# Optimization experiments

Hardware: AMD Instinct MI355X
Metric: run time of the kernel (lower is better)

## Reference

```python
import jax, jax.numpy as jnp
import numpy as np

OMODE, PMODE, NZ = 2, 4, 8
NY = NX = 512
NPY = NPX = 128
NPOS = 1024
BATCH = 64


def setup_inputs() -> dict:
    key = jax.random.key(0)
    ks = jax.random.split(key, 8)
    obja = jax.random.uniform(ks[0], (OMODE, NZ, NY, NX), jnp.float32, 0.9, 1.0)
    objp = 0.1 * jax.random.normal(ks[1], (OMODE, NZ, NY, NX), jnp.float32)
    probe = jax.random.normal(ks[2], (PMODE, NPY, NPX, 2), jnp.float32)
    probe_pos_shifts = 0.5 * jax.random.normal(ks[3], (NPOS, 2), jnp.float32)
    theta = jax.random.normal(ks[4], (NPY, NPX), jnp.float32)
    H = jnp.stack([jnp.cos(theta), jnp.sin(theta)], axis=-1)  # unit-modulus Fresnel phasor (re, im)
    omode_occu = jax.nn.softmax(jax.random.normal(ks[5], (OMODE,), jnp.float32))
    indices = jax.random.randint(ks[6], (BATCH,), 0, NPOS, jnp.int32)
    crop_pos = jax.random.randint(ks[7], (NPOS, 2), 0, NY - NPY, jnp.int32)
    return {"obja": obja, "objp": objp, "probe": probe,
            "probe_pos_shifts": probe_pos_shifts, "H": H, "omode_occu": omode_occu,
            "indices": indices, "crop_pos": crop_pos}


def reference(obja, objp, probe, probe_pos_shifts, H, omode_occu, indices, crop_pos):
    npy, npx = probe.shape[1], probe.shape[2]
    probe_c = probe[..., 0] + 1j * probe[..., 1]   # (pmode, Npy, Npx) complex64
    H_c = H[..., 0] + 1j * H[..., 1]               # (Npy, Npx) complex64

    # --- indexed patch gather: (omode, nz, N, Npy, Npx) -> (N, omode, nz, Npy, Npx) ---
    cy = crop_pos[indices, 0]
    cx = crop_pos[indices, 1]
    gy = cy[:, None, None] + jnp.arange(npy, dtype=jnp.int32)[None, :, None]  # (N, Npy, 1)
    gx = cx[:, None, None] + jnp.arange(npx, dtype=jnp.int32)[None, None, :]  # (N, 1, Npx)
    pa = jnp.transpose(obja[:, :, gy, gx], (2, 0, 1, 3, 4))
    pp = jnp.transpose(objp[:, :, gy, gx], (2, 0, 1, 3, 4))
    T = pa * jnp.exp(1j * pp)  # transmission per slice, (N, omode, nz, Npy, Npx)

    # --- sub-pixel Fourier probe shifts (imshift_batch) ---
    kpy = jnp.fft.fftfreq(npy).astype(jnp.float32)
    kpx = jnp.fft.fftfreq(npx).astype(jnp.float32)
    sh = probe_pos_shifts[indices]  # (N, 2)
    ramp = jnp.exp(-2j * jnp.pi * (kpy[None, :, None] * sh[:, 0, None, None]
                                   + kpx[None, None, :] * sh[:, 1, None, None]))  # (N, Npy, Npx)
    probes = jnp.fft.ifft2(jnp.fft.fft2(probe_c)[None] * ramp[:, None])  # (N, pmode, Npy, Npx)

    # --- multislice propagation: psi (N, omode, pmode, Npy, Npx) ---
    psi = probes[:, None]
    nz = T.shape[2]
    for z in range(nz):
        psi = psi * T[:, :, z, None]
        if z < nz - 1:
            psi = jnp.fft.ifft2(jnp.fft.fft2(psi) * H_c)

    # --- far-field detector intensity, mode-incoherent sum ---
    dp = jnp.einsum('o,nopyx->nyx', omode_occu, jnp.abs(jnp.fft.fft2(psi)) ** 2)
    return dp
```

## Files before the change

### kernel.cpp

```cpp
#include <hip/hip_runtime.h>

static constexpr int OMODE = 2, PMODE = 4, NZ = 8;
static constexpr int NYX = 512;
static constexpr int NP  = 128;
static constexpr int BATCH = 64;
static constexpr int LSTR = 129;
static constexpr float INV_N2 = 1.0f / 16384.0f;

typedef float v2f __attribute__((ext_vector_type(2)));

__device__ __forceinline__ int br7(int x) { return (int)(__brev((unsigned)x) >> 25); }

__device__ __forceinline__ v2f splat2(float s) { return (v2f){s, s}; }
__device__ __forceinline__ v2f swapv(v2f v) { return __builtin_shufflevector(v, v, 1, 0); }
__device__ __forceinline__ v2f cmulv(v2f a, float br_, float bi_) {
  return a * splat2(br_) + swapv(a) * (v2f){-bi_, bi_};
}
__device__ __forceinline__ v2f cmulvv(v2f a, v2f b) {
  return a * splat2(b.x) + swapv(a) * (v2f){-b.y, b.y};
}

template<int CTRL>
__device__ __forceinline__ float dppf(float x) {
  int i = __float_as_int(x);
  int r = __builtin_amdgcn_update_dpp(i, i, CTRL, 0xF, 0xF, false);
  return __int_as_float(r);
}

struct Tw {
  float tc6, ts6;
  float g[6];
  float dwr[6], dwi[6];
};

template<int CTRL, int S>
__device__ __forceinline__ v2f bfly_dpp(v2f m, const Tw& tw) {
  v2f t = (v2f){dppf<CTRL>(m.x), dppf<CTRL>(m.y)};
  return t + splat2(tw.g[S]) * m;
}
template<int OFS, int S>
__device__ __forceinline__ v2f bfly_swz(v2f m, const Tw& tw) {
  v2f t;
  t.x = __int_as_float(__builtin_amdgcn_ds_swizzle(__float_as_int(m.x), OFS));
  t.y = __int_as_float(__builtin_amdgcn_ds_swizzle(__float_as_int(m.y), OFS));
  return t + splat2(tw.g[S]) * m;
}
__device__ __forceinline__ v2f bfly_bp32(v2f m, int bp32, float g5) {
  v2f t;
  t.x = __int_as_float(__builtin_amdgcn_ds_bpermute(bp32, __float_as_int(m.x)));
  t.y = __int_as_float(__builtin_amdgcn_ds_bpermute(bp32, __float_as_int(m.y)));
  return t + splat2(g5) * m;
}

template<int S> __device__ __forceinline__ v2f twd(v2f d, const Tw& tw) {
  return d * splat2(tw.dwr[S]) + swapv(d) * (v2f){-tw.dwi[S], tw.dwi[S]};
}
template<int S> __device__ __forceinline__ v2f twc(v2f a, const Tw& tw) {
  return a * splat2(tw.dwr[S]) + swapv(a) * (v2f){tw.dwi[S], -tw.dwi[S]};
}

__device__ __forceinline__ void dif128(v2f& A, v2f& B, const Tw& tw, int bp32) {
  {
    v2f d = A - B;
    A = A + B;
    B = d * splat2(tw.tc6) + swapv(d) * (v2f){tw.ts6, -tw.ts6};
  }
  A = twd<5>(bfly_bp32(A, bp32, tw.g[5]), tw);  B = twd<5>(bfly_bp32(B, bp32, tw.g[5]), tw);
  A = twd<4>(bfly_swz<0x401F, 4>(A, tw), tw);   B = twd<4>(bfly_swz<0x401F, 4>(B, tw), tw);
  A = twd<3>(bfly_swz<0x201F, 3>(A, tw), tw);   B = twd<3>(bfly_swz<0x201F, 3>(B, tw), tw);
  A = twd<2>(bfly_swz<0x101F, 2>(A, tw), tw);   B = twd<2>(bfly_swz<0x101F, 2>(B, tw), tw);
  A = twd<1>(bfly_dpp<0x4E, 1>(A, tw), tw);     B = twd<1>(bfly_dpp<0x4E, 1>(B, tw), tw);
  A = bfly_dpp<0xB1, 0>(A, tw);                 B = bfly_dpp<0xB1, 0>(B, tw);
}

__device__ __forceinline__ void dit128(v2f& A, v2f& B, const Tw& tw, int bp32) {
  A = bfly_dpp<0xB1, 0>(A, tw);                 B = bfly_dpp<0xB1, 0>(B, tw);
  A = bfly_dpp<0x4E, 1>(twc<1>(A, tw), tw);     B = bfly_dpp<0x4E, 1>(twc<1>(B, tw), tw);
  A = bfly_swz<0x101F, 2>(twc<2>(A, tw), tw);   B = bfly_swz<0x101F, 2>(twc<2>(B, tw), tw);
  A = bfly_swz<0x201F, 3>(twc<3>(A, tw), tw);   B = bfly_swz<0x201F, 3>(twc<3>(B, tw), tw);
  A = bfly_swz<0x401F, 4>(twc<4>(A, tw), tw);   B = bfly_swz<0x401F, 4>(twc<4>(B, tw), tw);
  A = bfly_bp32(twc<5>(A, tw), bp32, tw.g[5]);  B = bfly_bp32(twc<5>(B, tw), bp32, tw.g[5]);
  {
    v2f m = B * splat2(tw.tc6) + swapv(B) * (v2f){-tw.ts6, tw.ts6};
    B = A - m;
    A = A + m;
  }
}

__global__ void __launch_bounds__(256) init_hpre(const float* __restrict__ H,
                                                 float2* __restrict__ hp) {
  int i = blockIdx.x * blockDim.x + threadIdx.x;
  if (i >= NP * NP) return;
  int px = i >> 7, py = i & (NP - 1);
  int ky = br7(py), kx = br7(px);
  hp[px * NP + py] = make_float2(H[(ky * NP + kx) * 2 + 0] * INV_N2,
                                 H[(ky * NP + kx) * 2 + 1] * INV_N2);
}

__global__ void __launch_bounds__(256) init_ramp(const float* __restrict__ shifts,
                                                 const int* __restrict__ indices,
                                                 float2* __restrict__ rampy,
                                                 float2* __restrict__ rampx) {
  int i = blockIdx.x * blockDim.x + threadIdx.x;
  if (i >= 2 * BATCH * NP) return;
  int which = (i >= BATCH * NP) ? 1 : 0;
  int r = i - which * BATCH * NP;
  int n = r >> 7, slot = r & (NP - 1);
  int pos = indices[n];
  float sh = shifts[2 * pos + which];
  int k = br7(slot);
  float f = (float)(k < 64 ? k : k - 128) * (1.f / 128.f);
  float s, c;
  __sincosf(-6.28318530717959f * f * sh, &s, &c);
  if (!which) rampy[n * NP + slot] = make_float2(c * INV_N2, s * INV_N2);
  else        rampx[n * NP + slot] = make_float2(c, s);
}

__global__ void __launch_bounds__(256) init_T(const float* __restrict__ obja,
                                              const float* __restrict__ objp,
                                              float2* __restrict__ T) {
  int i = blockIdx.x * 256 + threadIdx.x;
  if (i >= OMODE * NZ * NYX * NYX) return;
  float a = obja[i], ph = objp[i];
  float s, c;
  __sincosf(ph, &s, &c);
  T[i] = make_float2(a * c, a * s);
}

__global__ void __launch_bounds__(256) reduce_dp(const float* __restrict__ part,
                                                 const float* __restrict__ occu,
                                                 float* __restrict__ dp) {
  int i = blockIdx.x * 256 + threadIdx.x;
  if (i >= BATCH * NP * NP) return;
  int n = i >> 14;
  int r = i & (NP * NP - 1);
  int ky = r >> 7, kx = r & (NP - 1);
  const float* b = part + ((size_t)n * 8 << 14) + (kx << 7) + ky;
  float w0 = occu[0], w1 = occu[1];
  float s = 0.f;
#pragma unroll
  for (int j = 0; j < 8; ++j) s = fmaf(b[(size_t)j << 14], (j < 4 ? w0 : w1), s);
  dp[i] = s;
}

__global__ void
__attribute__((amdgpu_flat_work_group_size(1024, 1024), amdgpu_waves_per_eu(4, 4)))
ptycho_chain(
    const float* __restrict__ obja, const float* __restrict__ objp,
    const float* __restrict__ probe, const float* __restrict__ shifts,
    const float* __restrict__ H, const float2* __restrict__ hpre,
    const float2* __restrict__ rampy, const float2* __restrict__ rampx,
    const float2* __restrict__ Tpre,
    const float* __restrict__ occu, const int* __restrict__ indices,
    const int* __restrict__ crop, float* __restrict__ dp,
    float* __restrict__ part, int mode_ws, int mode_T)
{
  extern __shared__ v2f fld[];

  const int blk  = blockIdx.x;
  const int n    = blk >> 3;
  const int o    = (blk >> 2) & 1;
  const int p    = blk & 3;
  const int tid  = threadIdx.x;
  const int wid  = tid >> 6;
  const int lane = tid & 63;
  const int bp32 = (lane ^ 32) << 2;

  const int   pos = indices[n];
  const int   cy  = crop[2 * pos + 0];
  const int   cx  = crop[2 * pos + 1];
  const float wocc = occu[o];

  Tw tw;
  tw.g[0] = ((lane >> 0) & 1) ? -1.f : 1.f;
#pragma unroll
  for (int s = 1; s < 6; ++s) {
    int h = 1 << s;
    int j = lane & (h - 1);
    float ang = 3.14159265358979f * (float)j / (float)h;
    float ts_, tc_;
    __sincosf(ang, &ts_, &tc_);
    bool up = (lane >> s) & 1;
    tw.g[s]   = up ? -1.f : 1.f;
    tw.dwr[s] = up ? tc_ : 1.f;
    tw.dwi[s] = up ? -ts_ : 0.f;
  }
  __sincosf(3.14159265358979f * (float)lane * (1.f / 64.f), &tw.ts6, &tw.tc6);

  const v2f* probe2 = (const v2f*)probe;
#pragma unroll 1
  for (int k0 = 0; k0 < 8; k0 += 4) {
    int r0 = wid * 8 + k0;
    v2f A[4], B[4];
#pragma unroll
    for (int kk = 0; kk < 4; ++kk) {
      A[kk] = probe2[(p * NP + r0 + kk) * NP + lane];
      B[kk] = probe2[(p * NP + r0 + kk) * NP + lane + 64];
    }
#pragma unroll
    for (int kk = 0; kk < 4; ++kk) dif128(A[kk], B[kk], tw, bp32);
#pragma unroll
    for (int kk = 0; kk < 4; ++kk) {
      fld[(r0 + kk) * LSTR + lane]      = A[kk];
      fld[(r0 + kk) * LSTR + lane + 64] = B[kk];
    }
  }
  __syncthreads();

  auto ramp_mul_fb = [&](v2f& A, v2f& B, int c) {
    float sh0v = shifts[2 * pos], sh1v = shifts[2 * pos + 1];
    int kxc = br7(c);
    float fx = (float)(kxc < 64 ? kxc : kxc - 128) * (1.f / 128.f);
    int ky0 = br7(lane);
    float fy0 = (float)(ky0 < 64 ? ky0 : ky0 - 128) * (1.f / 128.f);
    int ky1 = ky0 + 1;
    float fy1 = (float)(ky1 < 64 ? ky1 : ky1 - 128) * (1.f / 128.f);
    float com = fx * sh1v;
    float s0, c0_, s1, c1_;
    __sincosf(-6.28318530717959f * (fy0 * sh0v + com), &s0, &c0_);
    __sincosf(-6.28318530717959f * (fy1 * sh0v + com), &s1, &c1_);
    A = cmulv(A, c0_ * INV_N2, s0 * INV_N2);
    B = cmulv(B, c1_ * INV_N2, s1 * INV_N2);
  };
  auto h_mul_fb = [&](v2f& A, v2f& B, int c) {
    int kx = br7(c), ky0 = br7(lane);
    float hr0 = H[(ky0 * NP + kx) * 2], hi0 = H[(ky0 * NP + kx) * 2 + 1];
    float hr1 = H[((ky0 + 1) * NP + kx) * 2], hi1 = H[((ky0 + 1) * NP + kx) * 2 + 1];
    A = cmulv(A, hr0 * INV_N2, hi0 * INV_N2);
    B = cmulv(B, hr1 * INV_N2, hi1 * INV_N2);
  };

  auto cphase = [&](int mode) {
    v2f ry0, ry1;
    if (mode == 0 && mode_ws) {
      float2 t0 = rampy[n * NP + lane];
      float2 t1 = rampy[n * NP + lane + 64];
      ry0 = (v2f){t0.x, t0.y}; ry1 = (v2f){t1.x, t1.y};
    }
#pragma unroll 1
    for (int k0 = 0; k0 < 8; k0 += 4) {
      int c0 = wid * 8 + k0;
      float2 h0[4], h1[4], rx[4];
      if (mode == 1 && mode_ws) {
#pragma unroll
        for (int kk = 0; kk < 4; ++kk) {
          h0[kk] = hpre[(c0 + kk) * NP + lane];
          h1[kk] = hpre[(c0 + kk) * NP + lane + 64];
        }
      }
      if (mode == 0 && mode_ws) {
#pragma unroll
        for (int kk = 0; kk < 4; ++kk) rx[kk] = rampx[n * NP + c0 + kk];
      }
      v2f A[4], B[4];
#pragma unroll
      for (int kk = 0; kk < 4; ++kk) {
        A[kk] = fld[lane * LSTR + c0 + kk];
        B[kk] = fld[(lane + 64) * LSTR + c0 + kk];
      }
#pragma unroll
      for (int kk = 0; kk < 4; ++kk) dif128(A[kk], B[kk], tw, bp32);
      if (mode == 0) {
        if (mode_ws) {
#pragma unroll
          for (int kk = 0; kk < 4; ++kk) {
            v2f m;
            m = cmulv(ry0, rx[kk].x, rx[kk].y); A[kk] = cmulvv(A[kk], m);
            m = cmulv(ry1, rx[kk].x, rx[kk].y); B[kk] = cmulvv(B[kk], m);
          }
        } else {
#pragma unroll
          for (int kk = 0; kk < 4; ++kk) ramp_mul_fb(A[kk], B[kk], c0 + kk);
        }
      } else {
        if (mode_ws) {
#pragma unroll
          for (int kk = 0; kk < 4; ++kk) {
            A[kk] = cmulv(A[kk], h0[kk].x, h0[kk].y);
            B[kk] = cmulv(B[kk], h1[kk].x, h1[kk].y);
          }
        } else {
#pragma unroll
          for (int kk = 0; kk < 4; ++kk) h_mul_fb(A[kk], B[kk], c0 + kk);
        }
      }
#pragma unroll
      for (int kk = 0; kk < 4; ++kk) dit128(A[kk], B[kk], tw, bp32);
#pragma unroll
      for (int kk = 0; kk < 4; ++kk) {
        fld[lane * LSTR + c0 + kk]        = A[kk];
        fld[(lane + 64) * LSTR + c0 + kk] = B[kk];
      }
    }
    __syncthreads();
  };

  auto rphase = [&](int z) {
#pragma unroll 1
    for (int k0 = 0; k0 < 8; k0 += 4) {
      int r0 = wid * 8 + k0;
      size_t ob = ((size_t)(o * NZ + z) * NYX + (size_t)(cy + r0)) * NYX + cx;
      v2f A[4], B[4];
#pragma unroll
      for (int kk = 0; kk < 4; ++kk) {
        A[kk] = fld[(r0 + kk) * LSTR + lane];
        B[kk] = fld[(r0 + kk) * LSTR + lane + 64];
      }
      if (mode_T) {
        float2 t0[4], t1[4];
#pragma unroll
        for (int kk = 0; kk < 4; ++kk) {
          t0[kk] = Tpre[ob + (size_t)kk * NYX + lane];
          t1[kk] = Tpre[ob + (size_t)kk * NYX + lane + 64];
        }
#pragma unroll
        for (int kk = 0; kk < 4; ++kk) dit128(A[kk], B[kk], tw, bp32);
#pragma unroll
        for (int kk = 0; kk < 4; ++kk) {
          A[kk] = cmulv(A[kk], t0[kk].x, t0[kk].y);
          B[kk] = cmulv(B[kk], t1[kk].x, t1[kk].y);
        }
      } else {
        float pa0[4], ph0[4], pa1[4], ph1[4];
#pragma unroll
        for (int kk = 0; kk < 4; ++kk) {
          pa0[kk] = obja[ob + (size_t)kk * NYX + lane];
          ph0[kk] = objp[ob + (size_t)kk * NYX + lane];
          pa1[kk] = obja[ob + (size_t)kk * NYX + lane + 64];
          ph1[kk] = objp[ob + (size_t)kk * NYX + lane + 64];
        }
#pragma unroll
        for (int kk = 0; kk < 4; ++kk) dit128(A[kk], B[kk], tw, bp32);
#pragma unroll
        for (int kk = 0; kk < 4; ++kk) {
          float s, c;
          __sincosf(ph0[kk], &s, &c); A[kk] = cmulv(A[kk], pa0[kk] * c, pa0[kk] * s);
          __sincosf(ph1[kk], &s, &c); B[kk] = cmulv(B[kk], pa1[kk] * c, pa1[kk] * s);
        }
      }
#pragma unroll
      for (int kk = 0; kk < 4; ++kk) dif128(A[kk], B[kk], tw, bp32);
#pragma unroll
      for (int kk = 0; kk < 4; ++kk) {
        fld[(r0 + kk) * LSTR + lane]      = A[kk];
        fld[(r0 + kk) * LSTR + lane + 64] = B[kk];
      }
    }
    __syncthreads();
  };

  cphase(0);
  rphase(0);
#pragma unroll 1
  for (int z = 1; z < NZ; ++z) {
    cphase(1);
    rphase(z);
  }

#pragma unroll 1
  for (int k0 = 0; k0 < 8; k0 += 4) {
    int c0 = wid * 8 + k0;
    v2f A[4], B[4];
#pragma unroll
    for (int kk = 0; kk < 4; ++kk) {
      A[kk] = fld[lane * LSTR + c0 + kk];
      B[kk] = fld[(lane + 64) * LSTR + c0 + kk];
    }
#pragma unroll
    for (int kk = 0; kk < 4; ++kk) dif128(A[kk], B[kk], tw, bp32);
    int ky0 = br7(lane);
#pragma unroll
    for (int kk = 0; kk < 4; ++kk) {
      float m0 = fmaf(A[kk].x, A[kk].x, A[kk].y * A[kk].y);
      float m1 = fmaf(B[kk].x, B[kk].x, B[kk].y * B[kk].y);
      if (mode_ws) {
        size_t b0 = ((size_t)blk << 14) + (size_t)br7(c0 + kk) * NP;
        part[b0 + ky0]     = m0;
        part[b0 + ky0 + 1] = m1;
      } else {
        size_t base = ((size_t)n << 14);
        atomicAdd(&dp[base + (size_t)ky0 * NP + br7(c0 + kk)],       m0 * wocc);
        atomicAdd(&dp[base + (size_t)(ky0 + 1) * NP + br7(c0 + kk)], m1 * wocc);
      }
    }
  }
}

extern "C" void kernel_launch(void* const* d_in, const int* in_sizes, int n_in,
                              void* d_out, int out_size, void* d_ws, size_t ws_size,
                              hipStream_t stream) {
  const float* obja   = (const float*)d_in[0];
  const float* objp   = (const float*)d_in[1];
  const float* probe  = (const float*)d_in[2];
  const float* shifts = (const float*)d_in[3];
  const float* H      = (const float*)d_in[4];
  const float* occu   = (const float*)d_in[5];
  const int*   indices = (const int*)d_in[6];
  const int*   crop    = (const int*)d_in[7];
  float* dp = (float*)d_out;

  const size_t part_bytes  = (size_t)BATCH * OMODE * PMODE * NP * NP * sizeof(float);
  const size_t hpre_bytes  = (size_t)NP * NP * sizeof(float2);
  const size_t ramp_bytes  = (size_t)BATCH * NP * sizeof(float2);
  const size_t T_bytes     = (size_t)OMODE * NZ * NYX * NYX * sizeof(float2);
  const size_t need_ws = part_bytes + hpre_bytes + 2 * ramp_bytes;
  const size_t need_T  = need_ws + T_bytes;

  int mode_ws = (ws_size >= need_ws) ? 1 : 0;
  int mode_T  = (ws_size >= need_T) ? 1 : 0;
  float*  part  = (float*)d_ws;
  float2* hpre  = (float2*)((char*)d_ws + part_bytes);
  float2* rampy = (float2*)((char*)d_ws + part_bytes + hpre_bytes);
  float2* rampx = (float2*)((char*)d_ws + part_bytes + hpre_bytes + ramp_bytes);
  float2* Tpre  = (float2*)((char*)d_ws + need_ws);

  if (mode_ws) {
    hipLaunchKernelGGL(init_hpre, dim3((NP * NP + 255) / 256), dim3(256), 0,
                       stream, H, hpre);
    hipLaunchKernelGGL(init_ramp, dim3((2 * BATCH * NP + 255) / 256), dim3(256), 0,
                       stream, shifts, indices, rampy, rampx);
  } else {
    hipMemsetAsync(d_out, 0, (size_t)out_size * sizeof(float), stream);
  }
  if (mode_T) {
    hipLaunchKernelGGL(init_T, dim3((OMODE * NZ * NYX * NYX + 255) / 256), dim3(256),
                       0, stream, obja, objp, Tpre);
  }

  const int lds_bytes = NP * LSTR * (int)sizeof(float2);
  hipFuncSetAttribute((const void*)ptycho_chain,
                      hipFuncAttributeMaxDynamicSharedMemorySize, lds_bytes);
  hipLaunchKernelGGL(ptycho_chain, dim3(BATCH * OMODE * PMODE), dim3(1024),
                     lds_bytes, stream,
                     obja, objp, probe, shifts, H, hpre, rampy, rampx, Tpre,
                     occu, indices, crop, dp, part, mode_ws, mode_T);
  if (mode_ws) {
    hipLaunchKernelGGL(reduce_dp, dim3((BATCH * NP * NP + 255) / 256), dim3(256),
                       0, stream, part, occu, dp);
  }
}
```

Before: 376.6 us.

## Precompute shifted probes once per batch/pmode in a separate kernel

New measurement: 383.8 us. No clear change (+1.9%).

```diff
diff --git a/kernel.cpp b/kernel.cpp
--- a/kernel.cpp
+++ b/kernel.cpp
@@ -85,6 +85,23 @@
     B = A - m;
     A = A + m;
   }
+}
+
+__device__ __forceinline__ void init_tw(Tw& tw, int lane) {
+  tw.g[0] = (lane & 1) ? -1.f : 1.f;
+#pragma unroll
+  for (int s = 1; s < 6; ++s) {
+    int h = 1 << s;
+    int j = lane & (h - 1);
+    float ang = 3.14159265358979f * (float)j / (float)h;
+    float ts_, tc_;
+    __sincosf(ang, &ts_, &tc_);
+    bool up = (lane >> s) & 1;
+    tw.g[s]   = up ? -1.f : 1.f;
+    tw.dwr[s] = up ? tc_ : 1.f;
+    tw.dwi[s] = up ? -ts_ : 0.f;
+  }
+  __sincosf(3.14159265358979f * (float)lane * (1.f / 64.f), &tw.ts6, &tw.tc6);
 }
 
 __global__ void __launch_bounds__(256) init_hpre(const float* __restrict__ H,
@@ -145,15 +162,108 @@
 
 __global__ void
 __attribute__((amdgpu_flat_work_group_size(1024, 1024), amdgpu_waves_per_eu(4, 4)))
+shift_probe(const float* __restrict__ probe,
+            const float2* __restrict__ rampy, const float2* __restrict__ rampx,
+            float2* __restrict__ ps)
+{
+  extern __shared__ v2f fld[];
+  const int blk  = blockIdx.x;
+  const int n    = blk >> 2;
+  const int p    = blk & 3;
+  const int tid  = threadIdx.x;
+  const int wid  = tid >> 6;
+  const int lane = tid & 63;
+  const int bp32 = (lane ^ 32) << 2;
+
+  Tw tw;
+  init_tw(tw, lane);
+
+  const v2f* probe2 = (const v2f*)probe;
+#pragma unroll 1
+  for (int k0 = 0; k0 < 8; k0 += 4) {
+    int r0 = wid * 8 + k0;
+    v2f A[4], B[4];
+#pragma unroll
+    for (int kk = 0; kk < 4; ++kk) {
+      A[kk] = probe2[(p * NP + r0 + kk) * NP + lane];
+      B[kk] = probe2[(p * NP + r0 + kk) * NP + lane + 64];
+    }
+#pragma unroll
+    for (int kk = 0; kk < 4; ++kk) dif128(A[kk], B[kk], tw, bp32);
+#pragma unroll
+    for (int kk = 0; kk < 4; ++kk) {
+      fld[(r0 + kk) * LSTR + lane]      = A[kk];
+      fld[(r0 + kk) * LSTR + lane + 64] = B[kk];
+    }
+  }
+  __syncthreads();
+
+  {
+    float2 t0 = rampy[n * NP + lane];
+    float2 t1 = rampy[n * NP + lane + 64];
+    v2f ry0 = (v2f){t0.x, t0.y}, ry1 = (v2f){t1.x, t1.y};
+#pragma unroll 1
+    for (int k0 = 0; k0 < 8; k0 += 4) {
+      int c0 = wid * 8 + k0;
+      float2 rx[4];
+#pragma unroll
+      for (int kk = 0; kk < 4; ++kk) rx[kk] = rampx[n * NP + c0 + kk];
+      v2f A[4], B[4];
+#pragma unroll
+      for (int kk = 0; kk < 4; ++kk) {
+        A[kk] = fld[lane * LSTR + c0 + kk];
+        B[kk] = fld[(lane + 64) * LSTR + c0 + kk];
+      }
+#pragma unroll
+      for (int kk = 0; kk < 4; ++kk) dif128(A[kk], B[kk], tw, bp32);
+#pragma unroll
+      for (int kk = 0; kk < 4; ++kk) {
+        v2f m;
+        m = cmulv(ry0, rx[kk].x, rx[kk].y); A[kk] = cmulvv(A[kk], m);
+        m = cmulv(ry1, rx[kk].x, rx[kk].y); B[kk] = cmulvv(B[kk], m);
+      }
+#pragma unroll
+      for (int kk = 0; kk < 4; ++kk) dit128(A[kk], B[kk], tw, bp32);
+#pragma unroll
+      for (int kk = 0; kk < 4; ++kk) {
+        fld[lane * LSTR + c0 + kk]        = A[kk];
+        fld[(lane + 64) * LSTR + c0 + kk] = B[kk];
+      }
+    }
+    __syncthreads();
+  }
+
+  float2* out = ps + ((size_t)blk << 14);
+#pragma unroll 1
+  for (int k0 = 0; k0 < 8; k0 += 4) {
+    int r0 = wid * 8 + k0;
+    v2f A[4], B[4];
+#pragma unroll
+    for (int kk = 0; kk < 4; ++kk) {
+      A[kk] = fld[(r0 + kk) * LSTR + lane];
+      B[kk] = fld[(r0 + kk) * LSTR + lane + 64];
+    }
+#pragma unroll
+    for (int kk = 0; kk < 4; ++kk) dit128(A[kk], B[kk], tw, bp32);
+#pragma unroll
+    for (int kk = 0; kk < 4; ++kk) {
+      out[(r0 + kk) * NP + lane]      = make_float2(A[kk].x, A[kk].y);
+      out[(r0 + kk) * NP + lane + 64] = make_float2(B[kk].x, B[kk].y);
+    }
+  }
+}
+
+__global__ void
+__attribute__((amdgpu_flat_work_group_size(1024, 1024), amdgpu_waves_per_eu(4, 4)))
 ptycho_chain(
     const float* __restrict__ obja, const float* __restrict__ objp,
     const float* __restrict__ probe, const float* __restrict__ shifts,
     const float* __restrict__ H, const float2* __restrict__ hpre,
     const float2* __restrict__ rampy, const float2* __restrict__ rampx,
-    const float2* __restrict__ Tpre,
+    const float2* __restrict__ Tpre, const float2* __restrict__ Ps,
     const float* __restrict__ occu, const int* __restrict__ indices,
     const int* __restrict__ crop, float* __restrict__ dp,
-    float* __restrict__ part, int mode_ws, int mode_T)
+    float* __restrict__ part, int mode_ws, int mode_T, int mode_ps)
 {
   extern __shared__ v2f fld[];
 
@@ -172,40 +282,7 @@
   const float wocc = occu[o];
 
   Tw tw;
-  tw.g[0] = ((lane >> 0) & 1) ? -1.f : 1.f;
-#pragma unroll
-  for (int s = 1; s < 6; ++s) {
-    int h = 1 << s;
-    int j = lane & (h - 1);
-    float ang = 3.14159265358979f * (float)j / (float)h;
-    float ts_, tc_;
-    __sincosf(ang, &ts_, &tc_);
-    bool up = (lane >> s) & 1;
-    tw.g[s]   = up ? -1.f : 1.f;
-    tw.dwr[s] = up ? tc_ : 1.f;
-    tw.dwi[s] = up ? -ts_ : 0.f;
-  }
-  __sincosf(3.14159265358979f * (float)lane * (1.f / 64.f), &tw.ts6, &tw.tc6);
-
-  const v2f* probe2 = (const v2f*)probe;
-#pragma unroll 1
-  for (int k0 = 0; k0 < 8; k0 += 4) {
-    int r0 = wid * 8 + k0;
-    v2f A[4], B[4];
-#pragma unroll
-    for (int kk = 0; kk < 4; ++kk) {
-      A[kk] = probe2[(p * NP + r0 + kk) * NP + lane];
-      B[kk] = probe2[(p * NP + r0 + kk) * NP + lane + 64];
-    }
-#pragma unroll
-    for (int kk = 0; kk < 4; ++kk) dif128(A[kk], B[kk], tw, bp32);
-#pragma unroll
-    for (int kk = 0; kk < 4; ++kk) {
-      fld[(r0 + kk) * LSTR + lane]      = A[kk];
-      fld[(r0 + kk) * LSTR + lane + 64] = B[kk];
-    }
-  }
-  __syncthreads();
+  init_tw(tw, lane);
 
   auto ramp_mul_fb = [&](v2f& A, v2f& B, int c) {
     float sh0v = shifts[2 * pos], sh1v = shifts[2 * pos + 1];
@@ -313,8 +390,8 @@
           t0[kk] = Tpre[ob + (size_t)kk * NYX + lane];
           t1[kk] = Tpre[ob + (size_t)kk * NYX + lane + 64];
         }
-#pragma unroll
-        for (int kk = 0; kk < 4; ++kk) dit128(A[kk], B[kk], tw, bp32);
+        dit128(A[0], B[0], tw, bp32); dit128(A[1], B[1], tw, bp32);
+        dit128(A[2], B[2], tw, bp32); dit128(A[3], B[3], tw, bp32);
 #pragma unroll
         for (int kk = 0; kk < 4; ++kk) {
           A[kk] = cmulv(A[kk], t0[kk].x, t0[kk].y);
@@ -329,8 +406,8 @@
           pa1[kk] = obja[ob + (size_t)kk * NYX + lane + 64];
           ph1[kk] = objp[ob + (size_t)kk * NYX + lane + 64];
         }
-#pragma unroll
-        for (int kk = 0; kk < 4; ++kk) dit128(A[kk], B[kk], tw, bp32);
+        dit128(A[0], B[0], tw, bp32); dit128(A[1], B[1], tw, bp32);
+        dit128(A[2], B[2], tw, bp32); dit128(A[3], B[3], tw, bp32);
 #pragma unroll
         for (int kk = 0; kk < 4; ++kk) {
           float s, c;
@@ -349,8 +426,55 @@
     __syncthreads();
   };
 
-  cphase(0);
-  rphase(0);
+  if (mode_ps) {
+    const float2* psf = Ps + ((size_t)((n << 2) + p) << 14);
+#pragma unroll 1
+    for (int k0 = 0; k0 < 8; k0 += 4) {
+      int r0 = wid * 8 + k0;
+      size_t ob = ((size_t)(o * NZ + 0) * NYX + (size_t)(cy + r0)) * NYX + cx;
+      v2f A[4], B[4];
+#pragma unroll
+      for (int kk = 0; kk < 4; ++kk) {
+        float2 p0 = psf[(r0 + kk) * NP + lane];
+        float2 p1 = psf[(r0 + kk) * NP + lane + 64];
+        float2 t0 = Tpre[ob + (size_t)kk * NYX + lane];
+        float2 t1 = Tpre[ob + (size_t)kk * NYX + lane + 64];
+        A[kk] = cmulv((v2f){p0.x, p0.y}, t0.x, t0.y);
+        B[kk] = cmulv((v2f){p1.x, p1.y}, t1.x, t1.y);
+      }
+#pragma unroll
+      for (int kk = 0; kk < 4; ++kk) dif128(A[kk], B[kk], tw, bp32);
+#pragma unroll
+      for (int kk = 0; kk < 4; ++kk) {
+        fld[(r0 + kk) * LSTR + lane]      = A[kk];
+        fld[(r0 + kk) * LSTR + lane + 64] = B[kk];
+      }
+    }
+    __syncthreads();
+  } else {
+    const v2f* probe2 = (const v2f*)probe;
+#pragma unroll 1
+    for (int k0 = 0; k0 < 8; k0 += 4) {
+      int r0 = wid * 8 + k0;
+      v2f A[4], B[4];
+#pragma unroll
+      for (int kk = 0; kk < 4; ++kk) {
+        A[kk] = probe2[(p * NP + r0 + kk) * NP + lane];
+        B[kk] = probe2[(p * NP + r0 + kk) * NP + lane + 64];
+      }
+#pragma unroll
+      for (int kk = 0; kk < 4; ++kk) dif128(A[kk], B[kk], tw, bp32);
+#pragma unroll
+      for (int kk = 0; kk < 4; ++kk) {
+        fld[(r0 + kk) * LSTR + lane]      = A[kk];
+        fld[(r0 + kk) * LSTR + lane + 64] = B[kk];
+      }
+    }
+    __syncthreads();
+    cphase(0);
+    rphase(0);
+  }
+
 #pragma unroll 1
   for (int z = 1; z < NZ; ++z) {
     cphase(1);
@@ -403,16 +527,20 @@
   const size_t hpre_bytes  = (size_t)NP * NP * sizeof(float2);
   const size_t ramp_bytes  = (size_t)BATCH * NP * sizeof(float2);
   const size_t T_bytes     = (size_t)OMODE * NZ * NYX * NYX * sizeof(float2);
+  const size_t ps_bytes    = (size_t)BATCH * PMODE * NP * NP * sizeof(float2);
   const size_t need_ws = part_bytes + hpre_bytes + 2 * ramp_bytes;
   const size_t need_T  = need_ws + T_bytes;
+  const size_t need_ps = need_T + ps_bytes;
 
   int mode_ws = (ws_size >= need_ws) ? 1 : 0;
   int mode_T  = (ws_size >= need_T) ? 1 : 0;
+  int mode_ps = (ws_size >= need_ps) ? 1 : 0;
   float*  part  = (float*)d_ws;
   float2* hpre  = (float2*)((char*)d_ws + part_bytes);
   float2* rampy = (float2*)((char*)d_ws + part_bytes + hpre_bytes);
   float2* rampx = (float2*)((char*)d_ws + part_bytes + hpre_bytes + ramp_bytes);
   float2* Tpre  = (float2*)((char*)d_ws + need_ws);
+  float2* Ps    = (float2*)((char*)d_ws + need_T);
 
   if (mode_ws) {
     hipLaunchKernelGGL(init_hpre, dim3((NP * NP + 255) / 256), dim3(256), 0,
@@ -428,12 +556,19 @@
   }
 
   const int lds_bytes = NP * LSTR * (int)sizeof(float2);
+  if (mode_ps) {
+    hipFuncSetAttribute((const void*)shift_probe,
+                        hipFuncAttributeMaxDynamicSharedMemorySize, lds_bytes);
+    hipLaunchKernelGGL(shift_probe, dim3(BATCH * PMODE), dim3(1024),
+                       lds_bytes, stream, probe, rampy, rampx, Ps);
+  }
+
   hipFuncSetAttribute((const void*)ptycho_chain,
                       hipFuncAttributeMaxDynamicSharedMemorySize, lds_bytes);
   hipLaunchKernelGGL(ptycho_chain, dim3(BATCH * OMODE * PMODE), dim3(1024),
                      lds_bytes, stream,
-                     obja, objp, probe, shifts, H, hpre, rampy, rampx, Tpre,
-                     occu, indices, crop, dp, part, mode_ws, mode_T);
+                     obja, objp, probe, shifts, H, hpre, rampy, rampx, Tpre, Ps,
+                     occu, indices, crop, dp, part, mode_ws, mode_T, mode_ps);
   if (mode_ws) {
     hipLaunchKernelGGL(reduce_dp, dim3((BATCH * NP * NP + 255) / 256), dim3(256),
                        0, stream, part, occu, dp);
```
